# Kernel optimization log

Hardware: AMD Instinct MI355X
Metric: run time of the kernel (lower is better)

The kernel has to match this reference:

```python
import jax, jax.numpy as jnp
import numpy as np

N_NODES = 50000
N_EDGES = 1000000
N_GRAPHS = 256
ORIG = 92
ATOM = 64
NBR = 41
EPS = 1e-5


def _bn_train(h, gamma, beta):
    # BatchNorm1d in training mode: batch stats, biased variance
    mu = h.mean(axis=0)
    var = jnp.var(h, axis=0)
    return (h - mu) * jax.lax.rsqrt(var + EPS) * gamma + beta


def setup_inputs() -> dict:
    key = jax.random.key(0)
    ks = jax.random.split(key, 16)
    inp = {
        "x": jax.random.normal(ks[0], (N_NODES, ORIG), dtype=jnp.float32),
        "edge_attr": jax.random.normal(ks[1], (N_EDGES, NBR), dtype=jnp.float32),
        "lower_f": jax.random.normal(ks[2], (N_NODES, ATOM), dtype=jnp.float32),
        "edge_index": jax.random.randint(ks[3], (2, N_EDGES), 0, N_NODES, dtype=jnp.int32),
        "batch": jnp.sort(jax.random.randint(ks[4], (N_NODES,), 0, N_GRAPHS, dtype=jnp.int32)),
        # params
        "emb_W": jax.random.normal(ks[5], (ORIG, ATOM), dtype=jnp.float32) / np.sqrt(ORIG),
        "emb_b": jnp.zeros((ATOM,), dtype=jnp.float32),
        "fc_W": jax.random.normal(ks[6], (2 * ATOM + NBR, 2 * ATOM), dtype=jnp.float32) / np.sqrt(2 * ATOM + NBR),
        "fc_b": jnp.zeros((2 * ATOM,), dtype=jnp.float32),
        "bn1_g": jnp.ones((2 * ATOM,), dtype=jnp.float32),
        "bn1_b": jnp.zeros((2 * ATOM,), dtype=jnp.float32),
        "bn2_g": jnp.ones((ATOM,), dtype=jnp.float32),
        "bn2_b": jnp.zeros((ATOM,), dtype=jnp.float32),
        "att_W": jax.random.normal(ks[7], (ATOM, 1), dtype=jnp.float32) / np.sqrt(ATOM),
        "att_b": jnp.zeros((1,), dtype=jnp.float32),
        "out_W": jax.random.normal(ks[8], (ATOM, 1), dtype=jnp.float32) / np.sqrt(ATOM),
        "out_b": jnp.zeros((1,), dtype=jnp.float32),
    }
    return inp


def reference(x, edge_attr, lower_f, emb_W, emb_b, fc_W, fc_b, bn1_g, bn1_b,
              bn2_g, bn2_b, att_W, att_b, out_W, out_b, edge_index, batch):
    # embedding + lower-level features
    atom_fea = x @ emb_W + emb_b + lower_f  # [N, ATOM]

    # CGConv: gather endpoints, concat with edge features
    src, dst = edge_index[0], edge_index[1]
    total = jnp.concatenate([atom_fea[src], atom_fea[dst], edge_attr], axis=-1)  # [E, 2A+NBR]
    gated = _bn_train(total @ fc_W + fc_b, bn1_g, bn1_b)  # [E, 2A]
    nbr_filter, nbr_core = gated[:, :ATOM], gated[:, ATOM:]
    msg = jax.nn.sigmoid(nbr_filter) * jax.nn.softplus(nbr_core)  # [E, A]
    summed = jax.ops.segment_sum(msg, src, num_segments=N_NODES)  # [N, A]
    atom_out = _bn_train(summed, bn2_g, bn2_b)

    # SiLU + attentional aggregation per graph
    h = jax.nn.silu(atom_out)  # [N, A]
    logits = (h @ att_W + att_b)[:, 0]  # [N]
    seg_max = jax.ops.segment_max(logits, batch, num_segments=N_GRAPHS)
    e = jnp.exp(logits - seg_max[batch])
    denom = jax.ops.segment_sum(e, batch, num_segments=N_GRAPHS)
    alpha = e / denom[batch]  # [N]
    crys = jax.ops.segment_sum(alpha[:, None] * h, batch, num_segments=N_GRAPHS)  # [G, A]
    crys_fea = crys @ out_W + out_b  # [G, 1]
    return atom_out, crys_fea
```

## Files before the change

### kernel.cpp

```cpp
#include <hip/hip_runtime.h>
#include <math.h>

#define NN 50000
#define NE 1000000
#define NG 256
#define ORIGD 92
#define NBRD 41
#define NSPREAD 32
#define SCAN_B 256

typedef unsigned short u16;
typedef __attribute__((ext_vector_type(8))) short short8;
typedef __attribute__((ext_vector_type(4))) float f32x4;

#define OFF_AFB     0
#define OFF_SUMMED  1600000
#define OFF_WT      4800000
#define OFF_BN1SPR  4812288
#define OFF_BN1SC   4820480
#define OFF_BN2ACC  4820736
#define OFF_BN2SC   4820864
#define OFF_ELOG    4820992
#define OFF_SEGMAX  4870992
#define OFF_DENOM   4871248
#define OFF_CNT     4871504
#define OFF_PTR     4921504
#define OFF_HEAD    4971504
#define OFF_BSUM    5021504
#define OFF_BOFS    5021760
#define OFF_EIDX    5022016
#define OFF_H       6022016
#define OFF_T2_END  70022016
#define OFF_P       70022016
#define OFF_T3_END  82822016
#define OFF_SRCC    82822016
#define OFF_DSTC    83822016
#define OFF_EAB     84822016
#define OFF_T4_END  108822016

__device__ __forceinline__ u16 f2b(float f) {
    unsigned u = __float_as_uint(f);
    return (u16)((u + 0x7FFFu + ((u >> 16) & 1u)) >> 16);
}
__device__ __forceinline__ float b2f(u16 u) {
    return __uint_as_float(((unsigned)u) << 16);
}
__device__ __forceinline__ float gate(float f, float cc) {
    float sig = __builtin_amdgcn_rcpf(1.f + __expf(-f));
    float sp  = fmaxf(cc, 0.f) + __logf(1.f + __expf(-fabsf(cc)));
    return sig * sp;
}
__device__ __forceinline__ float fsilu(float x) {
    return x * __builtin_amdgcn_rcpf(1.f + __expf(-x));
}

__global__ __launch_bounds__(256) void k_embed(
    const float* __restrict__ x, const float* __restrict__ lf,
    const float* __restrict__ W, const float* __restrict__ b,
    u16* __restrict__ afb)
{
    int gid = blockIdx.x * 256 + threadIdx.x;
    int n = gid >> 6, c = gid & 63;
    const float* xr = x + (long)n * ORIGD;
    float acc = b[c] + lf[gid];
#pragma unroll 4
    for (int k = 0; k < ORIGD; k++)
        acc = fmaf(xr[k], W[k * 64 + c], acc);
    afb[gid] = f2b(acc);
}

__global__ void k_prepw(const float* __restrict__ fcW, u16* __restrict__ wT)
{
    int i = blockIdx.x * 256 + threadIdx.x;
    int j = i / 192, k = i - j * 192;
    wT[i] = (k < 169) ? f2b(fcW[k * 128 + j]) : (u16)0;
}

__global__ void k_prepw2(const float* __restrict__ fcW, u16* __restrict__ wT3,
                         u16* __restrict__ wP)
{
    int i = blockIdx.x * 256 + threadIdx.x;
    if (i < 8192) {
        int j = i >> 6, k = i & 63;
        wT3[i] = (k < NBRD) ? f2b(fcW[(128 + k) * 128 + j]) : (u16)0;
    } else {
        int i2 = i - 8192;
        int j = i2 >> 6, k = i2 & 63;
        int row = (j < 128) ? k : (64 + k);
        wP[i2] = f2b(fcW[row * 128 + (j & 127)]);
    }
}

__global__ __launch_bounds__(256) void k_prepea(const float* __restrict__ ea,
                                                u16* __restrict__ eaB)
{
    int gid = blockIdx.x * 256 + threadIdx.x;
    if (gid >= NE * 6) return;
    int e = gid / 6, q = gid - e * 6;
    const float* row = ea + (long)e * NBRD;
    int c0 = q * 8;
    short8 v;
#pragma unroll
    for (int j = 0; j < 8; j++) {
        int c = c0 + j;
        v[j] = (c < NBRD) ? (short)f2b(row[c]) : (short)0;
    }
    *(short8*)(eaB + (long)e * 48 + c0) = v;
}

__global__ __launch_bounds__(256) void k_pnode(
    const u16* __restrict__ afb, const u16* __restrict__ wP, float* __restrict__ P)
{
    __shared__ __align__(16) u16 sB[64 * 72];
    const int tid = threadIdx.x;
    const int n0 = blockIdx.x * 64;

    for (int i = tid; i < 512; i += 256) {
        int r = i >> 3, c = i & 7;
        int n = n0 + r;
        short8 v = {0,0,0,0,0,0,0,0};
        if (n < NN) v = *(const short8*)(afb + (long)n * 64 + c * 8);
        *(short8*)(sB + r * 72 + c * 8) = v;
    }
    __syncthreads();

    const int lane = tid & 63, w = tid >> 6;
    const int n16 = lane & 15, quad = lane >> 4;
    short8 A[4][2];
#pragma unroll
    for (int m = 0; m < 4; m++) {
        const u16* base = wP + (16 * (w + 4 * m) + n16) * 64 + quad * 8;
        A[m][0] = *(const short8*)(base);
        A[m][1] = *(const short8*)(base + 32);
    }
    for (int t = 0; t < 4; t++) {
        const u16* row = sB + (16 * t + n16) * 72 + quad * 8;
        short8 b0 = *(const short8*)(row);
        short8 b1 = *(const short8*)(row + 32);
        int n = n0 + 16 * t + n16;
#pragma unroll
        for (int m = 0; m < 4; m++) {
            f32x4 acc = {0.f, 0.f, 0.f, 0.f};
            acc = __builtin_amdgcn_mfma_f32_16x16x32_bf16(A[m][0], b0, acc, 0, 0, 0);
            acc = __builtin_amdgcn_mfma_f32_16x16x32_bf16(A[m][1], b1, acc, 0, 0, 0);
            if (n < NN) {
                int j = 16 * (w + 4 * m) + 4 * quad;
                *(f32x4*)(P + (long)n * 256 + j) = acc;
            }
        }
    }
}

__global__ void k_hist(const int* __restrict__ ei, int* __restrict__ cnt)
{
    int e = blockIdx.x * 256 + threadIdx.x;
    if (e < NE) atomicAdd(&cnt[ei[e]], 1);
}

__global__ void k_partial(const int* __restrict__ cnt, int* __restrict__ lofs,
                          int* __restrict__ bsum)
{
    __shared__ int sd[SCAN_B];
    int t = threadIdx.x, b = blockIdx.x, n = b * SCAN_B + t;
    int v = (n < NN) ? cnt[n] : 0;
    sd[t] = v; __syncthreads();
    for (int o = 1; o < SCAN_B; o <<= 1) {
        int x = (t >= o) ? sd[t - o] : 0;
        __syncthreads();
        sd[t] += x;
        __syncthreads();
    }
    if (n < NN) lofs[n] = sd[t] - v;
    if (t == SCAN_B - 1) bsum[b] = sd[t];
}

__global__ void k_scanb(const int* __restrict__ bsum, int* __restrict__ bofs, int nb)
{
    __shared__ int sd[256];
    int t = threadIdx.x;
    int v = (t < nb) ? bsum[t] : 0;
    sd[t] = v; __syncthreads();
    for (int o = 1; o < 256; o <<= 1) {
        int x = (t >= o) ? sd[t - o] : 0;
        __syncthreads();
        sd[t] += x;
        __syncthreads();
    }
    bofs[t] = sd[t] - v;
}

__global__ void k_addofs(int* __restrict__ ptr, const int* __restrict__ bofs,
                         int* __restrict__ head)
{
    int n = blockIdx.x * 256 + threadIdx.x;
    if (n < NN) {
        int p = ptr[n] + bofs[n >> 8];
        ptr[n] = p; head[n] = p;
    }
}

__global__ void k_fill(const int* __restrict__ ei, int* __restrict__ head,
                       int* __restrict__ eidx)
{
    int e = blockIdx.x * 256 + threadIdx.x;
    if (e < NE) {
        int pos = atomicAdd(&head[ei[e]], 1);
        eidx[pos] = e;
    }
}

__global__ void k_fill2(const int* __restrict__ ei, int* __restrict__ head,
                        int* __restrict__ eidx, int* __restrict__ srcC,
                        int* __restrict__ dstC)
{
    int e = blockIdx.x * 256 + threadIdx.x;
    if (e < NE) {
        int s = ei[e];
        int pos = atomicAdd(&head[s], 1);
        eidx[pos] = e;
        srcC[pos] = s;
        dstC[pos] = ei[NE + e];
    }
}

__global__ __launch_bounds__(256) void k_gemm_h3(
    const u16* __restrict__ eaB, const int* __restrict__ eidx,
    const int* __restrict__ srcC, const int* __restrict__ dstC,
    const u16* __restrict__ wT3, const float* __restrict__ P,
    u16* __restrict__ h, float* __restrict__ spread)
{
    const int tid = threadIdx.x;
    const int e0 = blockIdx.x * 64;
    const int lane = tid & 63, w = tid >> 6;
    const int n16 = lane & 15, quad = lane >> 4;

    short8 A0[2], A1[2];
    {
        const u16* a0 = wT3 + (16 * w + n16) * 64 + quad * 8;
        const u16* a1 = wT3 + (16 * (w + 4) + n16) * 64 + quad * 8;
        A0[0] = *(const short8*)(a0);  A0[1] = *(const short8*)(a0 + 32);
        A1[0] = *(const short8*)(a1);  A1[1] = *(const short8*)(a1 + 32);
    }

    const int j0 = 16 * w + 4 * quad;
    const short8 bz = {0,0,0,0,0,0,0,0};
    float s0[4] = {0,0,0,0}, q0[4] = {0,0,0,0}, s1[4] = {0,0,0,0}, q1[4] = {0,0,0,0};

    for (int t = 0; t < 4; t++) {
        const int pos = e0 + 16 * t + n16;
        const int e   = eidx[pos];
        const int src = srcC[pos];
        const int dst = dstC[pos];

        const u16* er = eaB + (long)e * 48;
        short8 b0 = *(const short8*)(er + quad * 8);
        short8 b1 = bz;
        if (quad < 2) b1 = *(const short8*)(er + 32 + quad * 8);

        const float* pS = P + (long)src * 256;
        const float* pD = P + (long)dst * 256 + 128;
        f32x4 g0 = *(const f32x4*)(pS + j0);
        f32x4 g1 = *(const f32x4*)(pS + 64 + j0);
        f32x4 g2 = *(const f32x4*)(pD + j0);
        f32x4 g3 = *(const f32x4*)(pD + 64 + j0);

        f32x4 acc0 = {0.f, 0.f, 0.f, 0.f}, acc1 = {0.f, 0.f, 0.f, 0.f};
        acc0 = __builtin_amdgcn_mfma_f32_16x16x32_bf16(A0[0], b0, acc0, 0, 0, 0);
        acc0 = __builtin_amdgcn_mfma_f32_16x16x32_bf16(A0[1], b1, acc0, 0, 0, 0);
        acc1 = __builtin_amdgcn_mfma_f32_16x16x32_bf16(A1[0], b0, acc1, 0, 0, 0);
        acc1 = __builtin_amdgcn_mfma_f32_16x16x32_bf16(A1[1], b1, acc1, 0, 0, 0);

        u16 hv0[4], hv1[4];
#pragma unroll
        for (int r = 0; r < 4; r++) {
            float u0 = acc0[r] + g0[r] + g2[r];
            float u1 = acc1[r] + g1[r] + g3[r];
            s0[r] += u0; q0[r] = fmaf(u0, u0, q0[r]);
            s1[r] += u1; q1[r] = fmaf(u1, u1, q1[r]);
            hv0[r] = f2b(u0); hv1[r] = f2b(u1);
        }
        u16* hp = h + (long)pos * 128 + j0;
        ushort4 v0 = make_ushort4(hv0[0], hv0[1], hv0[2], hv0[3]);
        ushort4 v1 = make_ushort4(hv1[0], hv1[1], hv1[2], hv1[3]);
        *(ushort4*)hp = v0;
        *(ushort4*)(hp + 64) = v1;
    }

#pragma unroll
    for (int m = 1; m < 16; m <<= 1) {
#pragma unroll
        for (int r = 0; r < 4; r++) {
            s0[r] += __shfl_xor(s0[r], m); q0[r] += __shfl_xor(q0[r], m);
            s1[r] += __shfl_xor(s1[r], m); q1[r] += __shfl_xor(q1[r], m);
        }
    }
    if (n16 == 0) {
        float* sp = spread + (blockIdx.x & (NSPREAD - 1)) * 256;
#pragma unroll
        for (int r = 0; r < 4; r++) {
            atomicAdd(sp + j0 + r,       s0[r]);
            atomicAdd(sp + 128 + j0 + r, q0[r]);
            atomicAdd(sp + 64 + j0 + r,  s1[r]);
            atomicAdd(sp + 192 + j0 + r, q1[r]);
        }
    }
}

__global__ __launch_bounds__(256) void k_gemm_h2(
    const float* __restrict__ ea, const int* __restrict__ ei,
    const u16* __restrict__ wT3, const float* __restrict__ P,
    u16* __restrict__ h, float* __restrict__ spread)
{
    __shared__ __align__(16) u16 sTl[64 * 72];
    __shared__ int sSrc[64], sDst[64];
    const int tid = threadIdx.x;
    const int e0 = blockIdx.x * 64;

    if (tid < 64) sSrc[tid] = ei[e0 + tid];
    else if (tid < 128) sDst[tid - 64] = ei[NE + e0 + tid - 64];

    for (int i = tid; i < 64 * 64; i += 256) {
        int e = i >> 6, c = i & 63;
        float v = (c < NBRD) ? ea[(long)(e0 + e) * NBRD + c] : 0.f;
        sTl[e * 72 + c] = f2b(v);
    }
    __syncthreads();

    const int lane = tid & 63, w = tid >> 6;
    const int n16 = lane & 15, quad = lane >> 4;

    short8 A0[2], A1[2];
    {
        const u16* b0 = wT3 + (16 * w + n16) * 64 + quad * 8;
        const u16* b1 = wT3 + (16 * (w + 4) + n16) * 64 + quad * 8;
        A0[0] = *(const short8*)(b0);  A0[1] = *(const short8*)(b0 + 32);
        A1[0] = *(const short8*)(b1);  A1[1] = *(const short8*)(b1 + 32);
    }

    const int j0 = 16 * w + 4 * quad;
    float s0[4] = {0,0,0,0}, q0[4] = {0,0,0,0}, s1[4] = {0,0,0,0}, q1[4] = {0,0,0,0};

    for (int t = 0; t < 4; t++) {
        const int ge16 = 16 * t + n16;
        const int src = sSrc[ge16], dst = sDst[ge16];
        const float* pS = P + (long)src * 256;
        const float* pD = P + (long)dst * 256 + 128;
        f32x4 g0 = *(const f32x4*)(pS + j0);
        f32x4 g1 = *(const f32x4*)(pS + 64 + j0);
        f32x4 g2 = *(const f32x4*)(pD + j0);
        f32x4 g3 = *(const f32x4*)(pD + 64 + j0);

        const u16* row = sTl + ge16 * 72 + quad * 8;
        short8 b0 = *(const short8*)(row);
        short8 b1 = *(const short8*)(row + 32);
        f32x4 acc0 = {0.f, 0.f, 0.f, 0.f}, acc1 = {0.f, 0.f, 0.f, 0.f};
        acc0 = __builtin_amdgcn_mfma_f32_16x16x32_bf16(A0[0], b0, acc0, 0, 0, 0);
        acc0 = __builtin_amdgcn_mfma_f32_16x16x32_bf16(A0[1], b1, acc0, 0, 0, 0);
        acc1 = __builtin_amdgcn_mfma_f32_16x16x32_bf16(A1[0], b0, acc1, 0, 0, 0);
        acc1 = __builtin_amdgcn_mfma_f32_16x16x32_bf16(A1[1], b1, acc1, 0, 0, 0);

        u16 hv0[4], hv1[4];
#pragma unroll
        for (int r = 0; r < 4; r++) {
            float u0 = acc0[r] + g0[r] + g2[r];
            float u1 = acc1[r] + g1[r] + g3[r];
            s0[r] += u0; q0[r] = fmaf(u0, u0, q0[r]);
            s1[r] += u1; q1[r] = fmaf(u1, u1, q1[r]);
            hv0[r] = f2b(u0); hv1[r] = f2b(u1);
        }
        int ge = e0 + ge16;
        u16* hp = h + (long)ge * 128 + j0;
        ushort4 v0 = make_ushort4(hv0[0], hv0[1], hv0[2], hv0[3]);
        ushort4 v1 = make_ushort4(hv1[0], hv1[1], hv1[2], hv1[3]);
        *(ushort4*)hp = v0;
        *(ushort4*)(hp + 64) = v1;
    }

#pragma unroll
    for (int m = 1; m < 16; m <<= 1) {
#pragma unroll
        for (int r = 0; r < 4; r++) {
            s0[r] += __shfl_xor(s0[r], m); q0[r] += __shfl_xor(q0[r], m);
            s1[r] += __shfl_xor(s1[r], m); q1[r] += __shfl_xor(q1[r], m);
        }
    }
    if (n16 == 0) {
        float* sp = spread + (blockIdx.x & (NSPREAD - 1)) * 256;
#pragma unroll
        for (int r = 0; r < 4; r++) {
            atomicAdd(sp + j0 + r,       s0[r]);
            atomicAdd(sp + 128 + j0 + r, q0[r]);
            atomicAdd(sp + 64 + j0 + r,  s1[r]);
            atomicAdd(sp + 192 + j0 + r, q1[r]);
        }
    }
}

__global__ __launch_bounds__(256) void k_gemm_h(
    const u16* __restrict__ afb, const float* __restrict__ ea,
    const int* __restrict__ ei, const u16* __restrict__ wT,
    u16* __restrict__ h, float* __restrict__ spread)
{
    __shared__ __align__(16) u16 sTl[64 * 200];
    __shared__ int sSrc[64], sDst[64];
    const int tid = threadIdx.x;
    const int e0 = blockIdx.x * 64;

    if (tid < 64) sSrc[tid] = ei[e0 + tid];
    else if (tid < 128) sDst[tid - 64] = ei[NE + e0 + tid - 64];
    __syncthreads();

    for (int i = tid; i < 1024; i += 256) {
        int e = i >> 4, q = i & 15;
        const u16* g = (q < 8) ? (afb + (long)sSrc[e] * 64 + q * 8)
                               : (afb + (long)sDst[e] * 64 + (q - 8) * 8);
        *(short8*)(sTl + e * 200 + q * 8) = *(const short8*)g;
    }
    for (int i = tid; i < 64 * 64; i += 256) {
        int e = i >> 6, c = i & 63;
        float v = (c < NBRD) ? ea[(long)(e0 + e) * NBRD + c] : 0.f;
        sTl[e * 200 + 128 + c] = f2b(v);
    }
    __syncthreads();

    const int lane = tid & 63, w = tid >> 6;
    const int n16 = lane & 15, quad = lane >> 4;

    short8 A0[6], A1[6];
    {
        const u16* b0 = wT + (16 * w + n16) * 192 + quad * 8;
        const u16* b1 = wT + (16 * (w + 4) + n16) * 192 + quad * 8;
#pragma unroll
        for (int ks = 0; ks < 6; ks++) {
            A0[ks] = *(const short8*)(b0 + ks * 32);
            A1[ks] = *(const short8*)(b1 + ks * 32);
        }
    }

    const int j0 = 16 * w + 4 * quad;
    float s0[4] = {0,0,0,0}, q0[4] = {0,0,0,0}, s1[4] = {0,0,0,0}, q1[4] = {0,0,0,0};

    for (int t = 0; t < 4; t++) {
        const u16* row = sTl + (16 * t + n16) * 200 + quad * 8;
        f32x4 acc0 = {0.f, 0.f, 0.f, 0.f}, acc1 = {0.f, 0.f, 0.f, 0.f};
#pragma unroll
        for (int ks = 0; ks < 6; ks++) {
            short8 b = *(const short8*)(row + ks * 32);
            acc0 = __builtin_amdgcn_mfma_f32_16x16x32_bf16(A0[ks], b, acc0, 0, 0, 0);
            acc1 = __builtin_amdgcn_mfma_f32_16x16x32_bf16(A1[ks], b, acc1, 0, 0, 0);
        }
#pragma unroll
        for (int r = 0; r < 4; r++) {
            s0[r] += acc0[r]; q0[r] = fmaf(acc0[r], acc0[r], q0[r]);
            s1[r] += acc1[r]; q1[r] = fmaf(acc1[r], acc1[r], q1[r]);
        }
        int ge = e0 + 16 * t + n16;
        u16* hp = h + (long)ge * 128 + j0;
        ushort4 v0 = make_ushort4(f2b(acc0[0]), f2b(acc0[1]), f2b(acc0[2]), f2b(acc0[3]));
        ushort4 v1 = make_ushort4(f2b(acc1[0]), f2b(acc1[1]), f2b(acc1[2]), f2b(acc1[3]));
        *(ushort4*)hp = v0;
        *(ushort4*)(hp + 64) = v1;
    }

#pragma unroll
    for (int m = 1; m < 16; m <<= 1) {
#pragma unroll
        for (int r = 0; r < 4; r++) {
            s0[r] += __shfl_xor(s0[r], m); q0[r] += __shfl_xor(q0[r], m);
            s1[r] += __shfl_xor(s1[r], m); q1[r] += __shfl_xor(q1[r], m);
        }
    }
    if (n16 == 0) {
        float* sp = spread + (blockIdx.x & (NSPREAD - 1)) * 256;
#pragma unroll
        for (int r = 0; r < 4; r++) {
            atomicAdd(sp + j0 + r,       s0[r]);
            atomicAdd(sp + 128 + j0 + r, q0[r]);
            atomicAdd(sp + 64 + j0 + r,  s1[r]);
            atomicAdd(sp + 192 + j0 + r, q1[r]);
        }
    }
}

template <int MODE>
__global__ __launch_bounds__(256) void k_gemm(
    const u16* __restrict__ afb, const float* __restrict__ ea,
    const int* __restrict__ ei, const u16* __restrict__ wT,
    const float* __restrict__ sc, float* __restrict__ outbuf)
{
    __shared__ __align__(16) u16 sTl[64 * 200];
    __shared__ int sSrc[64], sDst[64];
    const int tid = threadIdx.x;
    const int e0 = blockIdx.x * 64;

    if (tid < 64) sSrc[tid] = ei[e0 + tid];
    else if (tid < 128) sDst[tid - 64] = ei[NE + e0 + tid - 64];
    __syncthreads();
    for (int i = tid; i < 1024; i += 256) {
        int e = i >> 4, q = i & 15;
        const u16* g = (q < 8) ? (afb + (long)sSrc[e] * 64 + q * 8)
                               : (afb + (long)sDst[e] * 64 + (q - 8) * 8);
        *(short8*)(sTl + e * 200 + q * 8) = *(const short8*)g;
    }
    for (int i = tid; i < 64 * 64; i += 256) {
        int e = i >> 6, c = i & 63;
        float v = (c < NBRD) ? ea[(long)(e0 + e) * NBRD + c] : 0.f;
        sTl[e * 200 + 128 + c] = f2b(v);
    }
    __syncthreads();

    const int lane = tid & 63, w = tid >> 6;
    const int n16 = lane & 15, quad = lane >> 4;
    short8 A0[6], A1[6];
    {
        const u16* b0 = wT + (16 * w + n16) * 192 + quad * 8;
        const u16* b1 = wT + (16 * (w + 4) + n16) * 192 + quad * 8;
#pragma unroll
        for (int ks = 0; ks < 6; ks++) {
            A0[ks] = *(const short8*)(b0 + ks * 32);
            A1[ks] = *(const short8*)(b1 + ks * 32);
        }
    }
    const int j0 = 16 * w + 4 * quad;
    float s0[4] = {0,0,0,0}, q0[4] = {0,0,0,0}, s1[4] = {0,0,0,0}, q1[4] = {0,0,0,0};
    float scf[4], shf[4], scc[4], shc[4];
    if (MODE == 1) {
#pragma unroll
        for (int r = 0; r < 4; r++) {
            scf[r] = sc[j0 + r];        shf[r] = sc[128 + j0 + r];
            scc[r] = sc[64 + j0 + r];   shc[r] = sc[192 + j0 + r];
        }
    }
    for (int t = 0; t < 4; t++) {
        const u16* row = sTl + (16 * t + n16) * 200 + quad * 8;
        f32x4 acc0 = {0.f, 0.f, 0.f, 0.f}, acc1 = {0.f, 0.f, 0.f, 0.f};
#pragma unroll
        for (int ks = 0; ks < 6; ks++) {
            short8 b = *(const short8*)(row + ks * 32);
            acc0 = __builtin_amdgcn_mfma_f32_16x16x32_bf16(A0[ks], b, acc0, 0, 0, 0);
            acc1 = __builtin_amdgcn_mfma_f32_16x16x32_bf16(A1[ks], b, acc1, 0, 0, 0);
        }
        if (MODE == 0) {
#pragma unroll
            for (int r = 0; r < 4; r++) {
                s0[r] += acc0[r]; q0[r] = fmaf(acc0[r], acc0[r], q0[r]);
                s1[r] += acc1[r]; q1[r] = fmaf(acc1[r], acc1[r], q1[r]);
            }
        } else {
            int src = sSrc[16 * t + n16];
            float* dst = outbuf + (long)src * 64 + j0;
#pragma unroll
            for (int r = 0; r < 4; r++) {
                float f  = fmaf(acc0[r], scf[r], shf[r]);
                float cc = fmaf(acc1[r], scc[r], shc[r]);
                atomicAdd(dst + r, gate(f, cc));
            }
        }
    }
    if (MODE == 0) {
#pragma unroll
        for (int m = 1; m < 16; m <<= 1) {
#pragma unroll
            for (int r = 0; r < 4; r++) {
                s0[r] += __shfl_xor(s0[r], m); q0[r] += __shfl_xor(q0[r], m);
                s1[r] += __shfl_xor(s1[r], m); q1[r] += __shfl_xor(q1[r], m);
            }
        }
        if (n16 == 0) {
            float* sp = outbuf + (blockIdx.x & (NSPREAD - 1)) * 256;
#pragma unroll
            for (int r = 0; r < 4; r++) {
                atomicAdd(sp + j0 + r,       s0[r]);
                atomicAdd(sp + 128 + j0 + r, q0[r]);
                atomicAdd(sp + 64 + j0 + r,  s1[r]);
                atomicAdd(sp + 192 + j0 + r, q1[r]);
            }
        }
    }
}

__global__ void k_bn1fin(const float* __restrict__ spread,
                         const float* __restrict__ g, const float* __restrict__ b,
                         float* __restrict__ sc)
{
    int c = threadIdx.x;
    float s = 0.f, q = 0.f;
    for (int k = 0; k < NSPREAD; k++) { s += spread[k * 256 + c]; q += spread[k * 256 + 128 + c]; }
    float mean_acc = s / (float)NE;
    float var = q / (float)NE - mean_acc * mean_acc;
    float scale = g[c] * rsqrtf(var + 1e-5f);
    sc[c] = scale;
    sc[128 + c] = b[c] - mean_acc * scale;
}

__global__ __launch_bounds__(256) void k_scatter2(
    const u16* __restrict__ h, const int* __restrict__ ptr,
    const int* __restrict__ cnt, const float* __restrict__ sc,
    float* __restrict__ summed)
{
    int tid = threadIdx.x;
    int n = blockIdx.x * 4 + (tid >> 6);
    int l = tid & 63;
    int es = l & 7, cg = l >> 3;

    float4 a0 = *(const float4*)(sc + cg * 8);
    float4 a1 = *(const float4*)(sc + cg * 8 + 4);
    float4 b0 = *(const float4*)(sc + 128 + cg * 8);
    float4 b1 = *(const float4*)(sc + 128 + cg * 8 + 4);
    float4 c0 = *(const float4*)(sc + 64 + cg * 8);
    float4 c1 = *(const float4*)(sc + 64 + cg * 8 + 4);
    float4 d0 = *(const float4*)(sc + 192 + cg * 8);
    float4 d1 = *(const float4*)(sc + 192 + cg * 8 + 4);
    float scf[8] = {a0.x,a0.y,a0.z,a0.w,a1.x,a1.y,a1.z,a1.w};
    float shf[8] = {b0.x,b0.y,b0.z,b0.w,b1.x,b1.y,b1.z,b1.w};
    float scc[8] = {c0.x,c0.y,c0.z,c0.w,c1.x,c1.y,c1.z,c1.w};
    float shc[8] = {d0.x,d0.y,d0.z,d0.w,d1.x,d1.y,d1.z,d1.w};

    int p0 = ptr[n], deg = cnt[n];
    float acc[8] = {0,0,0,0,0,0,0,0};
    for (int i = 0; i < deg; i += 8) {
        int idx = i + es;
        bool valid = idx < deg;
        int row = p0 + (valid ? idx : 0);
        const u16* hr = h + (long)row * 128;
        short8 f8 = *(const short8*)(hr + cg * 8);
        short8 c8 = *(const short8*)(hr + 64 + cg * 8);
#pragma unroll
        for (int j = 0; j < 8; j++) {
            float f  = fmaf(b2f((u16)f8[j]), scf[j], shf[j]);
            float cc = fmaf(b2f((u16)c8[j]), scc[j], shc[j]);
            float g  = gate(f, cc);
            acc[j] += valid ? g : 0.f;
        }
    }
#pragma unroll
    for (int m = 1; m < 8; m <<= 1)
#pragma unroll
        for (int j = 0; j < 8; j++) acc[j] += __shfl_xor(acc[j], m);
    if (es == 0) {
        float* sp = summed + (long)n * 64 + cg * 8;
        float4 v0 = {acc[0], acc[1], acc[2], acc[3]};
        float4 v1 = {acc[4], acc[5], acc[6], acc[7]};
        *(float4*)sp = v0;
        *(float4*)(sp + 4) = v1;
    }
}

__global__ __launch_bounds__(256) void k_scatter(
    const u16* __restrict__ h, const int* __restrict__ ptr,
    const int* __restrict__ cnt, const int* __restrict__ eidx,
    const float* __restrict__ sc, float* __restrict__ summed)
{
    int tid = threadIdx.x;
    int n = blockIdx.x * 4 + (tid >> 6);
    int l = tid & 63;
    int es = l & 7, cg = l >> 3;

    float4 a0 = *(const float4*)(sc + cg * 8);
    float4 a1 = *(const float4*)(sc + cg * 8 + 4);
    float4 b0 = *(const float4*)(sc + 128 + cg * 8);
    float4 b1 = *(const float4*)(sc + 128 + cg * 8 + 4);
    float4 c0 = *(const float4*)(sc + 64 + cg * 8);
    float4 c1 = *(const float4*)(sc + 64 + cg * 8 + 4);
    float4 d0 = *(const float4*)(sc + 192 + cg * 8);
    float4 d1 = *(const float4*)(sc + 192 + cg * 8 + 4);
    float scf[8] = {a0.x,a0.y,a0.z,a0.w,a1.x,a1.y,a1.z,a1.w};
    float shf[8] = {b0.x,b0.y,b0.z,b0.w,b1.x,b1.y,b1.z,b1.w};
    float scc[8] = {c0.x,c0.y,c0.z,c0.w,c1.x,c1.y,c1.z,c1.w};
    float shc[8] = {d0.x,d0.y,d0.z,d0.w,d1.x,d1.y,d1.z,d1.w};

    int p0 = ptr[n], deg = cnt[n];
    float acc[8] = {0,0,0,0,0,0,0,0};
    for (int i = 0; i < deg; i += 8) {
        int idx = i + es;
        bool valid = idx < deg;
        int e = eidx[p0 + (valid ? idx : 0)];
        const u16* hr = h + (long)e * 128;
        short8 f8 = *(const short8*)(hr + cg * 8);
        short8 c8 = *(const short8*)(hr + 64 + cg * 8);
#pragma unroll
        for (int j = 0; j < 8; j++) {
            float f  = fmaf(b2f((u16)f8[j]), scf[j], shf[j]);
            float cc = fmaf(b2f((u16)c8[j]), scc[j], shc[j]);
            float g  = gate(f, cc);
            acc[j] += valid ? g : 0.f;
        }
    }
#pragma unroll
    for (int m = 1; m < 8; m <<= 1)
#pragma unroll
        for (int j = 0; j < 8; j++) acc[j] += __shfl_xor(acc[j], m);
    if (es == 0) {
        float* sp = summed + (long)n * 64 + cg * 8;
        float4 v0 = {acc[0], acc[1], acc[2], acc[3]};
        float4 v1 = {acc[4], acc[5], acc[6], acc[7]};
        *(float4*)sp = v0;
        *(float4*)(sp + 4) = v1;
    }
}

__global__ __launch_bounds__(256) void k_bn2stats(const float* __restrict__ summed,
                                                  float* __restrict__ acc2)
{
    int tid = threadIdx.x; int c = tid & 63; int sub = tid >> 6;
    float s = 0.f, q = 0.f;
    for (int r = blockIdx.x * 4 + sub; r < NN; r += 4 * 128) {
        float v = summed[(long)r * 64 + c]; s += v; q = fmaf(v, v, q);
    }
    __shared__ float rs[256], rq[256];
    rs[tid] = s; rq[tid] = q; __syncthreads();
    if (tid < 64) {
        s = rs[tid] + rs[tid + 64] + rs[tid + 128] + rs[tid + 192];
        q = rq[tid] + rq[tid + 64] + rq[tid + 128] + rq[tid + 192];
        atomicAdd(&acc2[tid], s);
        atomicAdd(&acc2[64 + tid], q);
    }
}

__global__ void k_bn2fin(const float* __restrict__ acc2,
                         const float* __restrict__ g, const float* __restrict__ b,
                         float* __restrict__ sc2, const float* __restrict__ outb,
                         float* __restrict__ out)
{
    int c = threadIdx.x;
    if (c < 64) {
        float mean = acc2[c] / (float)NN;
        float var = acc2[64 + c] / (float)NN - mean * mean;
        float scale = g[c] * rsqrtf(var + 1e-5f);
        sc2[c] = scale;
        sc2[64 + c] = b[c] - mean * scale;
    }
    out[(long)NN * 64 + c] = outb[0];
}

__global__ __launch_bounds__(256) void k_nodepost(
    const float* __restrict__ summed, const float* __restrict__ sc2,
    const float* __restrict__ attW, const float* __restrict__ attb,
    const int* __restrict__ batch, float* __restrict__ out,
    float* __restrict__ elog, unsigned* __restrict__ segmax)
{
    int tid = threadIdx.x; int n = blockIdx.x * 4 + (tid >> 6); int c = tid & 63;
    float v = summed[(long)n * 64 + c];
    float ao = fmaf(v, sc2[c], sc2[64 + c]);
    out[(long)n * 64 + c] = ao;
    float h = fsilu(ao);
    float p = h * attW[c];
#pragma unroll
    for (int off = 32; off; off >>= 1) p += __shfl_down(p, off, 64);
    if (c == 0) {
        float logit = p + attb[0];
        elog[n] = logit;
        unsigned u = __float_as_uint(logit);
        u = (u & 0x80000000u) ? ~u : (u | 0x80000000u);
        atomicMax(&segmax[batch[n]], u);
    }
}

__global__ void k_denom(const int* __restrict__ batch,
                        const unsigned* __restrict__ segmax,
                        float* __restrict__ elog, float* __restrict__ denom)
{
    int n = blockIdx.x * 256 + threadIdx.x;
    if (n >= NN) return;
    int b = batch[n];
    unsigned u = segmax[b];
    u = (u & 0x80000000u) ? (u & 0x7FFFFFFFu) : ~u;
    float e = __expf(elog[n] - __uint_as_float(u));
    elog[n] = e;
    atomicAdd(&denom[b], e);
}

__global__ __launch_bounds__(256) void k_crys(
    const float* __restrict__ atom_out, const float* __restrict__ elog,
    const float* __restrict__ denom, const int* __restrict__ batch,
    const float* __restrict__ outW, float* __restrict__ out)
{
    int tid = threadIdx.x; int n = blockIdx.x * 4 + (tid >> 6); int l = tid & 63;
    int b = batch[n];
    float alpha = elog[n] / denom[b];
    float ao = atom_out[(long)n * 64 + l];
    float p = fsilu(ao) * outW[l];
#pragma unroll
    for (int off = 32; off; off >>= 1) p += __shfl_down(p, off, 64);
    if (l == 0) atomicAdd(&out[(long)NN * 64 + b], alpha * p);
}

extern "C" void kernel_launch(void* const* d_in, const int* in_sizes, int n_in,
                              void* d_out, int out_size, void* d_ws, size_t ws_size,
                              hipStream_t stream)
{
    const float* x    = (const float*)d_in[0];
    const float* eatt = (const float*)d_in[1];
    const float* lf   = (const float*)d_in[2];
    const int*   ei   = (const int*)d_in[3];
    const int*   batch= (const int*)d_in[4];
    const float* embW = (const float*)d_in[5];
    const float* embB = (const float*)d_in[6];
    const float* fcW  = (const float*)d_in[7];
    const float* bn1g = (const float*)d_in[9];
    const float* bn1b = (const float*)d_in[10];
    const float* bn2g = (const float*)d_in[11];
    const float* bn2b = (const float*)d_in[12];
    const float* attW = (const float*)d_in[13];
    const float* attB = (const float*)d_in[14];
    const float* outW = (const float*)d_in[15];
    const float* outB = (const float*)d_in[16];
    float* out = (float*)d_out;
    float* ws  = (float*)d_ws;

    u16* afb  = (u16*)(ws + OFF_AFB);
    u16* wT   = (u16*)(ws + OFF_WT);
    int* cnt  = (int*)(ws + OFF_CNT);
    int* ptr  = (int*)(ws + OFF_PTR);
    int* head = (int*)(ws + OFF_HEAD);
    int* bsum = (int*)(ws + OFF_BSUM);
    int* bofs = (int*)(ws + OFF_BOFS);
    int* eidx = (int*)(ws + OFF_EIDX);
    u16* h    = (u16*)(ws + OFF_H);

    const bool t4 = ws_size >= (size_t)OFF_T4_END * sizeof(float);
    const bool t3 = ws_size >= (size_t)OFF_T3_END * sizeof(float);
    const bool t2 = ws_size >= (size_t)OFF_T2_END * sizeof(float);

    k_embed<<<12500, 256, 0, stream>>>(x, lf, embW, embB, afb);

    if (t4) {
        u16* wT3  = wT;
        u16* wP   = wT + 8192;
        float* P  = ws + OFF_P;
        int* srcC = (int*)(ws + OFF_SRCC);
        int* dstC = (int*)(ws + OFF_DSTC);
        u16* eaB  = (u16*)(ws + OFF_EAB);
        k_prepw2<<<96, 256, 0, stream>>>(fcW, wT3, wP);
        hipMemsetAsync(ws + OFF_BN1SPR, 0,
                       (size_t)(OFF_PTR - OFF_BN1SPR) * sizeof(float), stream);
        k_prepea<<<(NE * 6 + 255) / 256, 256, 0, stream>>>(eatt, eaB);
        k_hist<<<(NE + 255) / 256, 256, 0, stream>>>(ei, cnt);
        k_partial<<<(NN + SCAN_B - 1) / SCAN_B, SCAN_B, 0, stream>>>(cnt, ptr, bsum);
        k_scanb<<<1, 256, 0, stream>>>(bsum, bofs, (NN + SCAN_B - 1) / SCAN_B);
        k_addofs<<<(NN + 255) / 256, 256, 0, stream>>>(ptr, bofs, head);
        k_fill2<<<(NE + 255) / 256, 256, 0, stream>>>(ei, head, eidx, srcC, dstC);
        k_pnode<<<(NN + 63) / 64, 256, 0, stream>>>(afb, wP, P);
        k_gemm_h3<<<NE / 64, 256, 0, stream>>>(eaB, eidx, srcC, dstC, wT3, P, h,
                                               ws + OFF_BN1SPR);
        k_bn1fin<<<1, 128, 0, stream>>>(ws + OFF_BN1SPR, bn1g, bn1b, ws + OFF_BN1SC);
        k_scatter2<<<NN / 4, 256, 0, stream>>>(h, ptr, cnt, ws + OFF_BN1SC,
                                               ws + OFF_SUMMED);
    } else if (t3) {
        u16* wT3 = wT;
        u16* wP  = wT + 8192;
        float* P = ws + OFF_P;
        k_prepw2<<<96, 256, 0, stream>>>(fcW, wT3, wP);
        hipMemsetAsync(ws + OFF_BN1SPR, 0,
                       (size_t)(OFF_PTR - OFF_BN1SPR) * sizeof(float), stream);
        k_hist<<<(NE + 255) / 256, 256, 0, stream>>>(ei, cnt);
        k_partial<<<(NN + SCAN_B - 1) / SCAN_B, SCAN_B, 0, stream>>>(cnt, ptr, bsum);
        k_scanb<<<1, 256, 0, stream>>>(bsum, bofs, (NN + SCAN_B - 1) / SCAN_B);
        k_addofs<<<(NN + 255) / 256, 256, 0, stream>>>(ptr, bofs, head);
        k_fill<<<(NE + 255) / 256, 256, 0, stream>>>(ei, head, eidx);
        k_pnode<<<(NN + 63) / 64, 256, 0, stream>>>(afb, wP, P);
        k_gemm_h2<<<NE / 64, 256, 0, stream>>>(eatt, ei, wT3, P, h, ws + OFF_BN1SPR);
        k_bn1fin<<<1, 128, 0, stream>>>(ws + OFF_BN1SPR, bn1g, bn1b, ws + OFF_BN1SC);
        k_scatter<<<NN / 4, 256, 0, stream>>>(h, ptr, cnt, eidx, ws + OFF_BN1SC,
                                              ws + OFF_SUMMED);
    } else if (t2) {
        k_prepw<<<96, 256, 0, stream>>>(fcW, wT);
        hipMemsetAsync(ws + OFF_BN1SPR, 0,
                       (size_t)(OFF_PTR - OFF_BN1SPR) * sizeof(float), stream);
        k_hist<<<(NE + 255) / 256, 256, 0, stream>>>(ei, cnt);
        k_partial<<<(NN + SCAN_B - 1) / SCAN_B, SCAN_B, 0, stream>>>(cnt, ptr, bsum);
        k_scanb<<<1, 256, 0, stream>>>(bsum, bofs, (NN + SCAN_B - 1) / SCAN_B);
        k_addofs<<<(NN + 255) / 256, 256, 0, stream>>>(ptr, bofs, head);
        k_fill<<<(NE + 255) / 256, 256, 0, stream>>>(ei, head, eidx);
        k_gemm_h<<<NE / 64, 256, 0, stream>>>(afb, eatt, ei, wT, h, ws + OFF_BN1SPR);
        k_bn1fin<<<1, 128, 0, stream>>>(ws + OFF_BN1SPR, bn1g, bn1b, ws + OFF_BN1SC);
        k_scatter<<<NN / 4, 256, 0, stream>>>(h, ptr, cnt, eidx, ws + OFF_BN1SC,
                                              ws + OFF_SUMMED);
    } else {
        k_prepw<<<96, 256, 0, stream>>>(fcW, wT);
        hipMemsetAsync(ws + OFF_SUMMED, 0,
                       (size_t)(OFF_PTR - OFF_SUMMED) * sizeof(float), stream);
        k_gemm<0><<<NE / 64, 256, 0, stream>>>(afb, eatt, ei, wT, ws + OFF_BN1SC,
                                               ws + OFF_BN1SPR);
        k_bn1fin<<<1, 128, 0, stream>>>(ws + OFF_BN1SPR, bn1g, bn1b, ws + OFF_BN1SC);
        k_gemm<1><<<NE / 64, 256, 0, stream>>>(afb, eatt, ei, wT, ws + OFF_BN1SC,
                                               ws + OFF_SUMMED);
    }

    k_bn2stats<<<128, 256, 0, stream>>>(ws + OFF_SUMMED, ws + OFF_BN2ACC);
    k_bn2fin<<<1, 256, 0, stream>>>(ws + OFF_BN2ACC, bn2g, bn2b, ws + OFF_BN2SC,
                                    outB, out);
    k_nodepost<<<12500, 256, 0, stream>>>(ws + OFF_SUMMED, ws + OFF_BN2SC, attW, attB,
                                          batch, out, ws + OFF_ELOG,
                                          (unsigned*)(ws + OFF_SEGMAX));
    k_denom<<<196, 256, 0, stream>>>(batch, (const unsigned*)(ws + OFF_SEGMAX),
                                     ws + OFF_ELOG, ws + OFF_DENOM);
    k_crys<<<12500, 256, 0, stream>>>(out, ws + OFF_ELOG, ws + OFF_DENOM, batch,
                                      outW, out);
}
```

Measured before the change: 1.212 ms.

## Fuse prep kernels, single-block scan, and fold edge-attr conversion into CSR fill

Merges weight prep and workspace zeroing into the embedding kernel, replaces the three-kernel prefix scan with one 1024-thread block, and moves the edge-attribute bf16 conversion into the CSR fill so edge features are written in sorted order. This drops the eidx indirection in the GEMM. The node projection P is stored in a packed layout so each lane reads 8 contiguous floats per endpoint, and the BN finalisation steps are folded into the scatter and node-post kernels. The aim is to cut launch count and memory passes. The cost is a scattered write of converted edge rows and some redundant BN-finalise work in every block.

Result: slower. 1.280 ms (+5.6%).

```diff
diff --git a/kernel.cpp b/kernel.cpp
--- a/kernel.cpp
+++ b/kernel.cpp
@@ -12,6 +12,7 @@
 typedef unsigned short u16;
 typedef __attribute__((ext_vector_type(8))) short short8;
 typedef __attribute__((ext_vector_type(4))) float f32x4;
+typedef __attribute__((ext_vector_type(8))) float f32x8;
 
 #define OFF_AFB     0
 #define OFF_SUMMED  1600000
@@ -54,10 +55,11 @@
     return x * __builtin_amdgcn_rcpf(1.f + __expf(-x));
 }
 
-__global__ __launch_bounds__(256) void k_embed(
+__global__ __launch_bounds__(256) void k_embed2(
     const float* __restrict__ x, const float* __restrict__ lf,
     const float* __restrict__ W, const float* __restrict__ b,
-    u16* __restrict__ afb)
+    u16* __restrict__ afb, const float* __restrict__ fcW,
+    u16* __restrict__ wT3, u16* __restrict__ wP, float* __restrict__ ws)
 {
     int gid = blockIdx.x * 256 + threadIdx.x;
     int n = gid >> 6, c = gid & 63;
@@ -67,6 +69,27 @@
     for (int k = 0; k < ORIGD; k++)
         acc = fmaf(xr[k], W[k * 64 + c], acc);
     afb[gid] = f2b(acc);
+
+    if (blockIdx.x < 96) {
+        int i = blockIdx.x * 256 + threadIdx.x;
+        if (i < 8192) {
+            int j = i >> 6, k = i & 63;
+            wT3[i] = (k < NBRD) ? f2b(fcW[(128 + k) * 128 + j]) : (u16)0;
+        } else {
+            int i2 = i - 8192;
+            int j = i2 >> 6, k = i2 & 63;
+            int row = (j < 128) ? k : (64 + k);
+            wP[i2] = f2b(fcW[row * 128 + (j & 127)]);
+        }
+    } else if (blockIdx.x < 336) {
+        int zid = (blockIdx.x - 96) * 256 + threadIdx.x;
+        if (zid < 8704) {
+            ws[OFF_BN1SPR + zid] = 0.f;
+        } else {
+            int z2 = zid - 8704;
+            if (z2 < 50512) ws[OFF_SEGMAX + z2] = 0.f;
+        }
+    }
 }
 
 __global__ void k_prepw(const float* __restrict__ fcW, u16* __restrict__ wT)
@@ -91,23 +114,22 @@
     }
 }
 
-__global__ __launch_bounds__(256) void k_prepea(const float* __restrict__ ea,
-                                                u16* __restrict__ eaB)
+__global__ __launch_bounds__(256) void k_embed(
+    const float* __restrict__ x, const float* __restrict__ lf,
+    const float* __restrict__ W, const float* __restrict__ b,
+    u16* __restrict__ afb)
 {
     int gid = blockIdx.x * 256 + threadIdx.x;
-    if (gid >= NE * 6) return;
-    int e = gid / 6, q = gid - e * 6;
-    const float* row = ea + (long)e * NBRD;
-    int c0 = q * 8;
-    short8 v;
-#pragma unroll
-    for (int j = 0; j < 8; j++) {
-        int c = c0 + j;
-        v[j] = (c < NBRD) ? (short)f2b(row[c]) : (short)0;
-    }
-    *(short8*)(eaB + (long)e * 48 + c0) = v;
-}
-
+    int n = gid >> 6, c = gid & 63;
+    const float* xr = x + (long)n * ORIGD;
+    float acc = b[c] + lf[gid];
+#pragma unroll 4
+    for (int k = 0; k < ORIGD; k++)
+        acc = fmaf(xr[k], W[k * 64 + c], acc);
+    afb[gid] = f2b(acc);
+}
+
+template <int PACKED>
 __global__ __launch_bounds__(256) void k_pnode(
     const u16* __restrict__ afb, const u16* __restrict__ wP, float* __restrict__ P)
 {
@@ -144,7 +166,14 @@
             acc = __builtin_amdgcn_mfma_f32_16x16x32_bf16(A[m][0], b0, acc, 0, 0, 0);
             acc = __builtin_amdgcn_mfma_f32_16x16x32_bf16(A[m][1], b1, acc, 0, 0, 0);
             if (n < NN) {
-                int j = 16 * (w + 4 * m) + 4 * quad;
+                int M = w + 4 * m;
+                int j;
+                if (PACKED) {
+                    int MM = M & 7;
+                    j = ((M >> 3) * 128) + ((MM & 3) * 4 + quad) * 8 + ((MM >> 2) << 2);
+                } else {
+                    j = 16 * M + 4 * quad;
+                }
                 *(f32x4*)(P + (long)n * 256 + j) = acc;
             }
         }
@@ -155,6 +184,39 @@
 {
     int e = blockIdx.x * 256 + threadIdx.x;
     if (e < NE) atomicAdd(&cnt[ei[e]], 1);
+}
+
+__global__ __launch_bounds__(1024) void k_scan1b(const int* __restrict__ cnt,
+                                                 int* __restrict__ ptr,
+                                                 int* __restrict__ head)
+{
+    __shared__ int sw[16];
+    const int t = threadIdx.x;
+    const int CH = (NN + 1023) / 1024;
+    const int base = t * CH;
+    int s = 0;
+    for (int i = 0; i < CH; i++) {
+        int n = base + i;
+        s += (n < NN) ? cnt[n] : 0;
+    }
+    int lane = t & 63, wv = t >> 6;
+    int v = s;
+    for (int o = 1; o < 64; o <<= 1) {
+        int x = __shfl_up(v, o, 64);
+        if (lane >= o) v += x;
+    }
+    if (lane == 63) sw[wv] = v;
+    __syncthreads();
+    if (t == 0) {
+        int acc = 0;
+        for (int i = 0; i < 16; i++) { int x = sw[i]; sw[i] = acc; acc += x; }
+    }
+    __syncthreads();
+    int p = sw[wv] + (v - s);
+    for (int i = 0; i < CH; i++) {
+        int n = base + i;
+        if (n < NN) { ptr[n] = p; head[n] = p; p += cnt[n]; }
+    }
 }
 
 __global__ void k_partial(const int* __restrict__ cnt, int* __restrict__ lofs,
@@ -209,25 +271,36 @@
     }
 }
 
-__global__ void k_fill2(const int* __restrict__ ei, int* __restrict__ head,
-                        int* __restrict__ eidx, int* __restrict__ srcC,
-                        int* __restrict__ dstC)
+__global__ __launch_bounds__(256) void k_fill3(
+    const int* __restrict__ ei, const float* __restrict__ ea,
+    int* __restrict__ head, int* __restrict__ srcC, int* __restrict__ dstC,
+    u16* __restrict__ eaB)
 {
     int e = blockIdx.x * 256 + threadIdx.x;
-    if (e < NE) {
-        int s = ei[e];
-        int pos = atomicAdd(&head[s], 1);
-        eidx[pos] = e;
-        srcC[pos] = s;
-        dstC[pos] = ei[NE + e];
-    }
-}
-
-__global__ __launch_bounds__(256) void k_gemm_h3(
-    const u16* __restrict__ eaB, const int* __restrict__ eidx,
-    const int* __restrict__ srcC, const int* __restrict__ dstC,
-    const u16* __restrict__ wT3, const float* __restrict__ P,
-    u16* __restrict__ h, float* __restrict__ spread)
+    if (e >= NE) return;
+    int s = ei[e];
+    int pos = atomicAdd(&head[s], 1);
+    srcC[pos] = s;
+    dstC[pos] = ei[NE + e];
+    const float* row = ea + (long)e * NBRD;
+    u16* orow = eaB + (long)pos * 48;
+#pragma unroll
+    for (int q = 0; q < 6; q++) {
+        short8 v;
+#pragma unroll
+        for (int j = 0; j < 8; j++) {
+            int c = q * 8 + j;
+            v[j] = (c < NBRD) ? (short)f2b(row[c]) : (short)0;
+        }
+        *(short8*)(orow + q * 8) = v;
+    }
+}
+
+__global__ __launch_bounds__(256) void k_gemm_h4(
+    const u16* __restrict__ eaB, const int* __restrict__ srcC,
+    const int* __restrict__ dstC, const u16* __restrict__ wT3,
+    const float* __restrict__ P, u16* __restrict__ h,
+    float* __restrict__ spread)
 {
     const int tid = threadIdx.x;
     const int e0 = blockIdx.x * 64;
@@ -243,26 +316,23 @@
     }
 
     const int j0 = 16 * w + 4 * quad;
+    const int pofs = (w * 4 + quad) * 8;
     const short8 bz = {0,0,0,0,0,0,0,0};
     float s0[4] = {0,0,0,0}, q0[4] = {0,0,0,0}, s1[4] = {0,0,0,0}, q1[4] = {0,0,0,0};
 
+#pragma unroll
     for (int t = 0; t < 4; t++) {
         const int pos = e0 + 16 * t + n16;
-        const int e   = eidx[pos];
         const int src = srcC[pos];
         const int dst = dstC[pos];
 
-        const u16* er = eaB + (long)e * 48;
+        const u16* er = eaB + (long)pos * 48;
         short8 b0 = *(const short8*)(er + quad * 8);
         short8 b1 = bz;
         if (quad < 2) b1 = *(const short8*)(er + 32 + quad * 8);
 
-        const float* pS = P + (long)src * 256;
-        const float* pD = P + (long)dst * 256 + 128;
-        f32x4 g0 = *(const f32x4*)(pS + j0);
-        f32x4 g1 = *(const f32x4*)(pS + 64 + j0);
-        f32x4 g2 = *(const f32x4*)(pD + j0);
-        f32x4 g3 = *(const f32x4*)(pD + 64 + j0);
+        f32x8 gS = *(const f32x8*)(P + (long)src * 256 + pofs);
+        f32x8 gD = *(const f32x8*)(P + (long)dst * 256 + 128 + pofs);
 
         f32x4 acc0 = {0.f, 0.f, 0.f, 0.f}, acc1 = {0.f, 0.f, 0.f, 0.f};
         acc0 = __builtin_amdgcn_mfma_f32_16x16x32_bf16(A0[0], b0, acc0, 0, 0, 0);
@@ -273,8 +343,8 @@
         u16 hv0[4], hv1[4];
 #pragma unroll
         for (int r = 0; r < 4; r++) {
-            float u0 = acc0[r] + g0[r] + g2[r];
-            float u1 = acc1[r] + g1[r] + g3[r];
+            float u0 = acc0[r] + gS[r] + gD[r];
+            float u1 = acc1[r] + gS[4 + r] + gD[4 + r];
             s0[r] += u0; q0[r] = fmaf(u0, u0, q0[r]);
             s1[r] += u1; q1[r] = fmaf(u1, u1, q1[r]);
             hv0[r] = f2b(u0); hv1[r] = f2b(u1);
@@ -593,10 +663,75 @@
     sc[128 + c] = b[c] - mean_acc * scale;
 }
 
-__global__ __launch_bounds__(256) void k_scatter2(
+__global__ __launch_bounds__(256) void k_scatter3(
     const u16* __restrict__ h, const int* __restrict__ ptr,
-    const int* __restrict__ cnt, const float* __restrict__ sc,
+    const int* __restrict__ cnt, const float* __restrict__ spread,
+    const float* __restrict__ g, const float* __restrict__ b,
     float* __restrict__ summed)
+{
+    __shared__ float ssc[256];
+    int tid = threadIdx.x;
+    if (tid < 128) {
+        int c = tid;
+        float s = 0.f, q = 0.f;
+        for (int k = 0; k < NSPREAD; k++) {
+            s += spread[k * 256 + c]; q += spread[k * 256 + 128 + c];
+        }
+        float mean_acc = s / (float)NE;
+        float var = q / (float)NE - mean_acc * mean_acc;
+        float scale = g[c] * rsqrtf(var + 1e-5f);
+        ssc[c] = scale;
+        ssc[128 + c] = b[c] - mean_acc * scale;
+    }
+    __syncthreads();
+
+    int n = blockIdx.x * 4 + (tid >> 6);
+    int l = tid & 63;
+    int es = l & 7, cg = l >> 3;
+
+    float scf[8], shf[8], scc[8], shc[8];
+#pragma unroll
+    for (int j = 0; j < 8; j++) {
+        scf[j] = ssc[cg * 8 + j];
+        shf[j] = ssc[128 + cg * 8 + j];
+        scc[j] = ssc[64 + cg * 8 + j];
+        shc[j] = ssc[192 + cg * 8 + j];
+    }
+
+    int p0 = ptr[n], deg = cnt[n];
+    float acc[8] = {0,0,0,0,0,0,0,0};
+    for (int i = 0; i < deg; i += 8) {
+        int idx = i + es;
+        bool valid = idx < deg;
+        int row = p0 + (valid ? idx : 0);
+        const u16* hr = h + (long)row * 128;
+        short8 f8 = *(const short8*)(hr + cg * 8);
+        short8 c8 = *(const short8*)(hr + 64 + cg * 8);
+#pragma unroll
+        for (int j = 0; j < 8; j++) {
+            float f  = fmaf(b2f((u16)f8[j]), scf[j], shf[j]);
+            float cc = fmaf(b2f((u16)c8[j]), scc[j], shc[j]);
+            float gg = gate(f, cc);
+            acc[j] += valid ? gg : 0.f;
+        }
+    }
+#pragma unroll
+    for (int m = 1; m < 8; m <<= 1)
+#pragma unroll
+        for (int j = 0; j < 8; j++) acc[j] += __shfl_xor(acc[j], m);
+    if (es == 0) {
+        float* sp = summed + (long)n * 64 + cg * 8;
+        float4 v0 = {acc[0], acc[1], acc[2], acc[3]};
+        float4 v1 = {acc[4], acc[5], acc[6], acc[7]};
+        *(float4*)sp = v0;
+        *(float4*)(sp + 4) = v1;
+    }
+}
+
+__global__ __launch_bounds__(256) void k_scatter(
+    const u16* __restrict__ h, const int* __restrict__ ptr,
+    const int* __restrict__ cnt, const int* __restrict__ eidx,
+    const float* __restrict__ sc, float* __restrict__ summed)
 {
     int tid = threadIdx.x;
     int n = blockIdx.x * 4 + (tid >> 6);
@@ -621,16 +756,16 @@
     for (int i = 0; i < deg; i += 8) {
         int idx = i + es;
         bool valid = idx < deg;
-        int row = p0 + (valid ? idx : 0);
-        const u16* hr = h + (long)row * 128;
+        int e = eidx[p0 + (valid ? idx : 0)];
+        const u16* hr = h + (long)e * 128;
         short8 f8 = *(const short8*)(hr + cg * 8);
         short8 c8 = *(const short8*)(hr + 64 + cg * 8);
 #pragma unroll
         for (int j = 0; j < 8; j++) {
             float f  = fmaf(b2f((u16)f8[j]), scf[j], shf[j]);
             float cc = fmaf(b2f((u16)c8[j]), scc[j], shc[j]);
-            float g  = gate(f, cc);
-            acc[j] += valid ? g : 0.f;
+            float gg = gate(f, cc);
+            acc[j] += valid ? gg : 0.f;
         }
     }
 #pragma unroll
@@ -646,59 +781,6 @@
     }
 }
 
-__global__ __launch_bounds__(256) void k_scatter(
-    const u16* __restrict__ h, const int* __restrict__ ptr,
-    const int* __restrict__ cnt, const int* __restrict__ eidx,
-    const float* __restrict__ sc, float* __restrict__ summed)
-{
-    int tid = threadIdx.x;
-    int n = blockIdx.x * 4 + (tid >> 6);
-    int l = tid & 63;
-    int es = l & 7, cg = l >> 3;
-
-    float4 a0 = *(const float4*)(sc + cg * 8);
-    float4 a1 = *(const float4*)(sc + cg * 8 + 4);
-    float4 b0 = *(const float4*)(sc + 128 + cg * 8);
-    float4 b1 = *(const float4*)(sc + 128 + cg * 8 + 4);
-    float4 c0 = *(const float4*)(sc + 64 + cg * 8);
-    float4 c1 = *(const float4*)(sc + 64 + cg * 8 + 4);
-    float4 d0 = *(const float4*)(sc + 192 + cg * 8);
-    float4 d1 = *(const float4*)(sc + 192 + cg * 8 + 4);
-    float scf[8] = {a0.x,a0.y,a0.z,a0.w,a1.x,a1.y,a1.z,a1.w};
-    float shf[8] = {b0.x,b0.y,b0.z,b0.w,b1.x,b1.y,b1.z,b1.w};
-    float scc[8] = {c0.x,c0.y,c0.z,c0.w,c1.x,c1.y,c1.z,c1.w};
-    float shc[8] = {d0.x,d0.y,d0.z,d0.w,d1.x,d1.y,d1.z,d1.w};
-
-    int p0 = ptr[n], deg = cnt[n];
-    float acc[8] = {0,0,0,0,0,0,0,0};
-    for (int i = 0; i < deg; i += 8) {
-        int idx = i + es;
-        bool valid = idx < deg;
-        int e = eidx[p0 + (valid ? idx : 0)];
-        const u16* hr = h + (long)e * 128;
-        short8 f8 = *(const short8*)(hr + cg * 8);
-        short8 c8 = *(const short8*)(hr + 64 + cg * 8);
-#pragma unroll
-        for (int j = 0; j < 8; j++) {
-            float f  = fmaf(b2f((u16)f8[j]), scf[j], shf[j]);
-            float cc = fmaf(b2f((u16)c8[j]), scc[j], shc[j]);
-            float g  = gate(f, cc);
-            acc[j] += valid ? g : 0.f;
-        }
-    }
-#pragma unroll
-    for (int m = 1; m < 8; m <<= 1)
-#pragma unroll
-        for (int j = 0; j < 8; j++) acc[j] += __shfl_xor(acc[j], m);
-    if (es == 0) {
-        float* sp = summed + (long)n * 64 + cg * 8;
-        float4 v0 = {acc[0], acc[1], acc[2], acc[3]};
-        float4 v1 = {acc[4], acc[5], acc[6], acc[7]};
-        *(float4*)sp = v0;
-        *(float4*)(sp + 4) = v1;
-    }
-}
-
 __global__ __launch_bounds__(256) void k_bn2stats(const float* __restrict__ summed,
                                                   float* __restrict__ acc2)
 {
@@ -733,15 +815,27 @@
     out[(long)NN * 64 + c] = outb[0];
 }
 
-__global__ __launch_bounds__(256) void k_nodepost(
-    const float* __restrict__ summed, const float* __restrict__ sc2,
+__global__ __launch_bounds__(256) void k_nodepost2(
+    const float* __restrict__ summed, const float* __restrict__ acc2,
+    const float* __restrict__ g, const float* __restrict__ b,
     const float* __restrict__ attW, const float* __restrict__ attb,
     const int* __restrict__ batch, float* __restrict__ out,
     float* __restrict__ elog, unsigned* __restrict__ segmax)
 {
-    int tid = threadIdx.x; int n = blockIdx.x * 4 + (tid >> 6); int c = tid & 63;
+    __shared__ float ssc2[128];
+    int tid = threadIdx.x;
+    if (tid < 64) {
+        float mean = acc2[tid] / (float)NN;
+        float var = acc2[64 + tid] / (float)NN - mean * mean;
+        float scale = g[tid] * rsqrtf(var + 1e-5f);
+        ssc2[tid] = scale;
+        ssc2[64 + tid] = b[tid] - mean * scale;
+    }
+    __syncthreads();
+
+    int n = blockIdx.x * 4 + (tid >> 6); int c = tid & 63;
     float v = summed[(long)n * 64 + c];
-    float ao = fmaf(v, sc2[c], sc2[64 + c]);
+    float ao = fmaf(v, ssc2[c], ssc2[64 + c]);
     out[(long)n * 64 + c] = ao;
     float h = fsilu(ao);
     float p = h * attW[c];
@@ -754,6 +848,45 @@
         u = (u & 0x80000000u) ? ~u : (u | 0x80000000u);
         atomicMax(&segmax[batch[n]], u);
     }
+}
+
+__global__ __launch_bounds__(256) void k_nodepost(
+    const float* __restrict__ summed, const float* __restrict__ sc2,
+    const float* __restrict__ attW, const float* __restrict__ attb,
+    const int* __restrict__ batch, float* __restrict__ out,
+    float* __restrict__ elog, unsigned* __restrict__ segmax)
+{
+    int tid = threadIdx.x; int n = blockIdx.x * 4 + (tid >> 6); int c = tid & 63;
+    float v = summed[(long)n * 64 + c];
+    float ao = fmaf(v, sc2[c], sc2[64 + c]);
+    out[(long)n * 64 + c] = ao;
+    float h = fsilu(ao);
+    float p = h * attW[c];
+#pragma unroll
+    for (int off = 32; off; off >>= 1) p += __shfl_down(p, off, 64);
+    if (c == 0) {
+        float logit = p + attb[0];
+        elog[n] = logit;
+        unsigned u = __float_as_uint(logit);
+        u = (u & 0x80000000u) ? ~u : (u | 0x80000000u);
+        atomicMax(&segmax[batch[n]], u);
+    }
+}
+
+__global__ void k_denom2(const int* __restrict__ batch,
+                         const unsigned* __restrict__ segmax,
+                         float* __restrict__ elog, float* __restrict__ denom,
+                         const float* __restrict__ outb, float* __restrict__ out)
+{
+    int n = blockIdx.x * 256 + threadIdx.x;
+    if (n < NG) out[(long)NN * 64 + n] = outb[0];
+    if (n >= NN) return;
+    int b = batch[n];
+    unsigned u = segmax[b];
+    u = (u & 0x80000000u) ? (u & 0x7FFFFFFFu) : ~u;
+    float e = __expf(elog[n] - __uint_as_float(u));
+    elog[n] = e;
+    atomicAdd(&denom[b], e);
 }
 
 __global__ void k_denom(const int* __restrict__ batch,
@@ -822,8 +955,6 @@
     const bool t3 = ws_size >= (size_t)OFF_T3_END * sizeof(float);
     const bool t2 = ws_size >= (size_t)OFF_T2_END * sizeof(float);
 
-    k_embed<<<12500, 256, 0, stream>>>(x, lf, embW, embB, afb);
-
     if (t4) {
         u16* wT3  = wT;
         u16* wP   = wT + 8192;
@@ -831,22 +962,30 @@
         int* srcC = (int*)(ws + OFF_SRCC);
         int* dstC = (int*)(ws + OFF_DSTC);
         u16* eaB  = (u16*)(ws + OFF_EAB);
-        k_prepw2<<<96, 256, 0, stream>>>(fcW, wT3, wP);
-        hipMemsetAsync(ws + OFF_BN1SPR, 0,
-                       (size_t)(OFF_PTR - OFF_BN1SPR) * sizeof(float), stream);
-        k_prepea<<<(NE * 6 + 255) / 256, 256, 0, stream>>>(eatt, eaB);
+        k_embed2<<<12500, 256, 0, stream>>>(x, lf, embW, embB, afb, fcW, wT3, wP, ws);
         k_hist<<<(NE + 255) / 256, 256, 0, stream>>>(ei, cnt);
-        k_partial<<<(NN + SCAN_B - 1) / SCAN_B, SCAN_B, 0, stream>>>(cnt, ptr, bsum);
-        k_scanb<<<1, 256, 0, stream>>>(bsum, bofs, (NN + SCAN_B - 1) / SCAN_B);
-        k_addofs<<<(NN + 255) / 256, 256, 0, stream>>>(ptr, bofs, head);
-        k_fill2<<<(NE + 255) / 256, 256, 0, stream>>>(ei, head, eidx, srcC, dstC);
-        k_pnode<<<(NN + 63) / 64, 256, 0, stream>>>(afb, wP, P);
-        k_gemm_h3<<<NE / 64, 256, 0, stream>>>(eaB, eidx, srcC, dstC, wT3, P, h,
+        k_scan1b<<<1, 1024, 0, stream>>>(cnt, ptr, head);
+        k_fill3<<<(NE + 255) / 256, 256, 0, stream>>>(ei, eatt, head, srcC, dstC, eaB);
+        k_pnode<1><<<(NN + 63) / 64, 256, 0, stream>>>(afb, wP, P);
+        k_gemm_h4<<<NE / 64, 256, 0, stream>>>(eaB, srcC, dstC, wT3, P, h,
                                                ws + OFF_BN1SPR);
-        k_bn1fin<<<1, 128, 0, stream>>>(ws + OFF_BN1SPR, bn1g, bn1b, ws + OFF_BN1SC);
-        k_scatter2<<<NN / 4, 256, 0, stream>>>(h, ptr, cnt, ws + OFF_BN1SC,
-                                               ws + OFF_SUMMED);
-    } else if (t3) {
+        k_scatter3<<<NN / 4, 256, 0, stream>>>(h, ptr, cnt, ws + OFF_BN1SPR,
+                                               bn1g, bn1b, ws + OFF_SUMMED);
+        k_bn2stats<<<128, 256, 0, stream>>>(ws + OFF_SUMMED, ws + OFF_BN2ACC);
+        k_nodepost2<<<12500, 256, 0, stream>>>(ws + OFF_SUMMED, ws + OFF_BN2ACC,
+                                               bn2g, bn2b, attW, attB, batch, out,
+                                               ws + OFF_ELOG,
+                                               (unsigned*)(ws + OFF_SEGMAX));
+        k_denom2<<<196, 256, 0, stream>>>(batch, (const unsigned*)(ws + OFF_SEGMAX),
+                                          ws + OFF_ELOG, ws + OFF_DENOM, outB, out);
+        k_crys<<<12500, 256, 0, stream>>>(out, ws + OFF_ELOG, ws + OFF_DENOM, batch,
+                                          outW, out);
+        return;
+    }
+
+    k_embed<<<12500, 256, 0, stream>>>(x, lf, embW, embB, afb);
+
+    if (t3) {
         u16* wT3 = wT;
         u16* wP  = wT + 8192;
         float* P = ws + OFF_P;
@@ -858,7 +997,7 @@
         k_scanb<<<1, 256, 0, stream>>>(bsum, bofs, (NN + SCAN_B - 1) / SCAN_B);
         k_addofs<<<(NN + 255) / 256, 256, 0, stream>>>(ptr, bofs, head);
         k_fill<<<(NE + 255) / 256, 256, 0, stream>>>(ei, head, eidx);
-        k_pnode<<<(NN + 63) / 64, 256, 0, stream>>>(afb, wP, P);
+        k_pnode<0><<<(NN + 63) / 64, 256, 0, stream>>>(afb, wP, P);
         k_gemm_h2<<<NE / 64, 256, 0, stream>>>(eatt, ei, wT3, P, h, ws + OFF_BN1SPR);
         k_bn1fin<<<1, 128, 0, stream>>>(ws + OFF_BN1SPR, bn1g, bn1b, ws + OFF_BN1SC);
         k_scatter<<<NN / 4, 256, 0, stream>>>(h, ptr, cnt, eidx, ws + OFF_BN1SC,
```
